# Kernel tuning notes

Hardware: AMD Instinct MI355X
Metric: run time of the kernel (lower is better)

## Reference

```python
import jax, jax.numpy as jnp
import numpy as np
import math

N_HEADS = 12
ROPE_DIM = 64
BASE = 10000.0


def _rope_tables(seq_len, dim):
    inv_freq = 1.0 / (BASE ** (jnp.arange(0, dim, 2, dtype=jnp.float32) / dim))
    t = jnp.arange(seq_len, dtype=jnp.float32)
    freqs = jnp.outer(t, inv_freq)                      # [S, dim/2]
    emb = jnp.concatenate([freqs, freqs], axis=-1)      # [S, dim]
    # broadcast shape [1, S, 1, dim]
    return jnp.cos(emb)[None, :, None, :], jnp.sin(emb)[None, :, None, :]


def _rotate_half(x):
    x1, x2 = jnp.split(x, 2, axis=-1)
    return jnp.concatenate([-x2, x1], axis=-1)


def setup_inputs() -> dict:
    key = jax.random.key(0)
    ks = jax.random.split(key, 9)
    B, S, E = 2, 2048, 768
    s = 1.0 / math.sqrt(E)
    return {
        "x": jax.random.normal(ks[0], (B, S, E), jnp.float32),
        "Wq": jax.random.normal(ks[1], (E, E), jnp.float32) * s,
        "bq": jax.random.normal(ks[2], (E,), jnp.float32) * 0.02,
        "Wk": jax.random.normal(ks[3], (E, E), jnp.float32) * s,
        "bk": jax.random.normal(ks[4], (E,), jnp.float32) * 0.02,
        "Wv": jax.random.normal(ks[5], (E, E), jnp.float32) * s,
        "bv": jax.random.normal(ks[6], (E,), jnp.float32) * 0.02,
        "Wp": jax.random.normal(ks[7], (E, E), jnp.float32) * s,
        "bp": jax.random.normal(ks[8], (E,), jnp.float32) * 0.02,
    }


def reference(x, Wq, bq, Wk, bk, Wv, bv, Wp, bp):
    B, S, E = x.shape
    H = N_HEADS
    D = E // H

    q = (x @ Wq + bq).reshape(B, S, H, D)
    k = (x @ Wk + bk).reshape(B, S, H, D)
    v = (x @ Wv + bv).reshape(B, S, H, D)

    # rotary on first ROPE_DIM dims (here ROPE_DIM == D, so full rotary)
    cos, sin = _rope_tables(S, ROPE_DIM)
    q_rot, q_pass = q[..., :ROPE_DIM], q[..., ROPE_DIM:]
    k_rot, k_pass = k[..., :ROPE_DIM], k[..., ROPE_DIM:]
    q_rot = q_rot * cos + _rotate_half(q_rot) * sin
    k_rot = k_rot * cos + _rotate_half(k_rot) * sin
    q = jnp.concatenate([q_rot, q_pass], axis=-1)
    k = jnp.concatenate([k_rot, k_pass], axis=-1)

    # scores [B, M, N, H]; mask before scaling (as in the torch code; -inf unchanged)
    att = jnp.einsum("bmhd,bnhd->bmnh", q, k)
    causal = jnp.tril(jnp.ones((S, S), dtype=bool))[None, :, :, None]
    att = jnp.where(causal, att, -jnp.inf)
    att = jax.nn.softmax(att / math.sqrt(D), axis=2)
    out = jnp.einsum("bmnh,bnhd->bmhd", att, v)

    return out.reshape(B, S, E) @ Wp + bp
```

## Files before the change

### kernel.cpp

```cpp
#include <hip/hip_runtime.h>
#include <stdint.h>

#define S_LEN 2048
#define EMB   768
#define NH    12
#define DH    64
#define M_TOT 4096
#define WELEM 589824
#define QELEM 3145728

typedef float  floatx4 __attribute__((ext_vector_type(4)));
typedef __bf16 bf16x8  __attribute__((ext_vector_type(8)));
typedef __bf16 bf16x4  __attribute__((ext_vector_type(4)));
typedef unsigned short ushortx4 __attribute__((ext_vector_type(4)));

__device__ __forceinline__ unsigned short f2bf(float f) {
    union { float f; unsigned u; } v; v.f = f;
    unsigned u = v.u;
    unsigned r = (u + 0x7FFFu + ((u >> 16) & 1u)) >> 16;
    return (unsigned short)r;
}

__device__ __forceinline__ void gl_lds16(const void* g, void* l) {
    __builtin_amdgcn_global_load_lds(
        (__attribute__((address_space(1))) const void*)g,
        (__attribute__((address_space(3))) void*)l, 16, 0, 0);
}

__global__ void cvt_all_kernel(const float* __restrict__ x, unsigned short* __restrict__ xb,
                               const float* __restrict__ W0, const float* __restrict__ W1,
                               const float* __restrict__ W2, const float* __restrict__ W3,
                               unsigned short* __restrict__ WT_all) {
    __shared__ float t[64][65];
    const int blk = blockIdx.x;
    if (blk < 3072) {
        int i = (blk * 256 + threadIdx.x) * 4;
        float4 v = *(const float4*)(x + i);
        ushortx4 r = { f2bf(v.x), f2bf(v.y), f2bf(v.z), f2bf(v.w) };
        *(ushortx4*)(xb + i) = r;
        return;
    }
    const int tc = blk - 3072;
    const int z = tc / 144, rr0 = tc % 144;
    const float* W = (z == 0) ? W0 : (z == 1 ? W1 : (z == 2 ? W2 : W3));
    unsigned short* O = WT_all + (size_t)z * WELEM;
    const int k0 = (rr0 % 12) * 64, n0 = (rr0 / 12) * 64;
    const int c = threadIdx.x & 63, r4 = threadIdx.x >> 6;
#pragma unroll
    for (int rr = 0; rr < 64; rr += 4) {
        int r = rr + r4;
        t[r][c] = W[(size_t)(k0 + r) * EMB + n0 + c];
    }
    __syncthreads();
#pragma unroll
    for (int rr = 0; rr < 64; rr += 4) {
        int nn = rr + r4;
        O[(size_t)(n0 + nn) * EMB + k0 + c] = f2bf(t[c][nn]);
    }
}

static __device__ __forceinline__ void gemm_core_128x128(
    const unsigned short* __restrict__ A, const unsigned short* __restrict__ BT,
    int m0, int n0, int K, int tid, floatx4 (&acc)[4][4],
    unsigned short* Als, unsigned short* Bls)
{
    const int lane = tid & 63;
    const int c0 = lane & 15, quad = lane >> 4;
    const int wave = tid >> 6;
    const int wm = (wave >> 1) * 64, wn = (wave & 1) * 64;

    for (int k0 = 0; k0 < K; k0 += 64) {
        __syncthreads();
#pragma unroll
        for (int it = 0; it < 4; ++it) {
            int ch = it * 256 + tid;
            int row = ch >> 3, sc = ch & 7;
            int cc = sc ^ (row & 7);
            gl_lds16(A  + (size_t)(m0 + row) * K + k0 + cc * 8, Als + ch * 8);
            gl_lds16(BT + (size_t)(n0 + row) * K + k0 + cc * 8, Bls + ch * 8);
        }
        __syncthreads();
        bf16x8 af[4][2], bfv[4][2];
#pragma unroll
        for (int ii = 0; ii < 4; ++ii) {
            int row = wm + 16 * ii + c0;
#pragma unroll
            for (int h = 0; h < 2; ++h)
                af[ii][h] = *(const bf16x8*)(Als + row * 64 + (((4 * h + quad) ^ (row & 7)) * 8));
        }
#pragma unroll
        for (int jj = 0; jj < 4; ++jj) {
            int row = wn + 16 * jj + c0;
#pragma unroll
            for (int h = 0; h < 2; ++h)
                bfv[jj][h] = *(const bf16x8*)(Bls + row * 64 + (((4 * h + quad) ^ (row & 7)) * 8));
        }
#pragma unroll
        for (int ii = 0; ii < 4; ++ii)
#pragma unroll
            for (int jj = 0; jj < 4; ++jj) {
                acc[ii][jj] = __builtin_amdgcn_mfma_f32_16x16x32_bf16(af[ii][0], bfv[jj][0], acc[ii][jj], 0, 0, 0);
                acc[ii][jj] = __builtin_amdgcn_mfma_f32_16x16x32_bf16(af[ii][1], bfv[jj][1], acc[ii][jj], 0, 0, 0);
            }
    }
}

__global__ __launch_bounds__(256, 2) void qkv_kernel(
    const unsigned short* __restrict__ xb, const unsigned short* __restrict__ WT_all,
    const float* __restrict__ bq, const float* __restrict__ bk, const float* __restrict__ bv,
    unsigned short* __restrict__ qkv_out)
{
    __shared__ __align__(16) unsigned short Als[128 * 64];
    __shared__ __align__(16) unsigned short Bls[128 * 64];
    const int z = blockIdx.z;
    const float* bias = (z == 0) ? bq : (z == 1 ? bk : bv);
    __bf16* Cout = (__bf16*)(qkv_out + (size_t)z * QELEM);
    const int m0 = blockIdx.x * 128, n0 = blockIdx.y * 128;
    const int tid = threadIdx.x, lane = tid & 63, c0 = lane & 15, quad = lane >> 4, wave = tid >> 6;
    const int wm = (wave >> 1) * 64, wn = (wave & 1) * 64;

    floatx4 acc[4][4] = {};
    gemm_core_128x128(xb, WT_all + (size_t)z * WELEM, m0, n0, EMB, tid, acc, Als, Bls);

#pragma unroll
    for (int ii = 0; ii < 4; ++ii) {
#pragma unroll
        for (int r = 0; r < 4; ++r) {
            int m = m0 + wm + 16 * ii + quad * 4 + r;
            int b = m >> 11, s = m & (S_LEN - 1);
            float vals[4];
#pragma unroll
            for (int jj = 0; jj < 4; ++jj) vals[jj] = acc[ii][jj][r] + bias[n0 + wn + 16 * jj + c0];
            if (z < 2) {
#pragma unroll
                for (int jj = 0; jj < 2; ++jj) {
                    int d = 16 * jj + c0;
                    float f = exp2f((float)d * -0.41524101186092034f);
                    float th = (float)s * f;
                    float sn, cs; sincosf(th, &sn, &cs);
                    float lo = vals[jj], hi = vals[jj + 2];
                    vals[jj]     = lo * cs - hi * sn;
                    vals[jj + 2] = hi * cs + lo * sn;
                }
            }
            if (z == 0) {
#pragma unroll
                for (int jj = 0; jj < 4; ++jj) vals[jj] *= 0.18033688011112042f;
            }
#pragma unroll
            for (int jj = 0; jj < 4; ++jj) {
                int n = n0 + wn + 16 * jj + c0;
                int h = n >> 6, d = n & 63;
                if (z < 2)
                    Cout[((size_t)(b * NH + h) * S_LEN + s) * DH + d] = (__bf16)vals[jj];
                else
                    Cout[((size_t)(b * NH + h) * DH + d) * S_LEN + s] = (__bf16)vals[jj];
            }
        }
    }
}

__global__ __launch_bounds__(256, 2) void flash_kernel(
    const unsigned short* __restrict__ Qg, const unsigned short* __restrict__ Kg,
    const unsigned short* __restrict__ Vt, unsigned short* __restrict__ Og)
{
    __shared__ __align__(16) unsigned short Kls[2][64 * 64];
    __shared__ __align__(16) unsigned short Vls[2][64 * 64];
    __shared__ __align__(16) unsigned short Pls[4][16 * 72];

    const int i = blockIdx.x;
    const int kk = i >> 8, g = i & 255;
    const int r0 = (kk == 0) ? g : (kk == 1 ? 511 - g : 512 + g);
    const int qt = 31 - r0 / 24;
    const int bh = r0 % 24;
    const int b = bh / NH, h = bh % NH;
    const int m0 = qt * 64;
    const int tid = threadIdx.x, lane = tid & 63, wave = tid >> 6;
    const int c0 = lane & 15, quad = lane >> 4;
    const size_t base = (size_t)bh * S_LEN * DH;
    const int mrow = m0 + wave * 16 + c0;

    bf16x8 qf0 = *(const bf16x8*)(Qg + base + (size_t)mrow * DH + quad * 8);
    bf16x8 qf1 = *(const bf16x8*)(Qg + base + (size_t)mrow * DH + 32 + quad * 8);

    floatx4 oa[4] = {};
    float l_lane = 0.f;
    const float C = 23.083120654223414f;
    const int ntiles = qt + 1;

#pragma unroll
    for (int it = 0; it < 2; ++it) {
        int ch = it * 256 + tid;
        int row = ch >> 3, cc = (ch & 7) ^ (row & 7);
        gl_lds16(Kg + base + (size_t)row * DH + cc * 8, &Kls[0][ch * 8]);
        gl_lds16(Vt + base + (size_t)row * S_LEN + cc * 8, &Vls[0][ch * 8]);
    }

    for (int nt = 0; nt < ntiles; ++nt) {
        __syncthreads();
        if (nt + 1 < ntiles) {
            int n0 = (nt + 1) * 64, buf = (nt + 1) & 1;
#pragma unroll
            for (int it = 0; it < 2; ++it) {
                int ch = it * 256 + tid;
                int row = ch >> 3, cc = (ch & 7) ^ (row & 7);
                gl_lds16(Kg + base + (size_t)(n0 + row) * DH + cc * 8, &Kls[buf][ch * 8]);
                gl_lds16(Vt + base + (size_t)row * S_LEN + n0 + cc * 8, &Vls[buf][ch * 8]);
            }
        }
        const unsigned short* Kb = Kls[nt & 1];
        const unsigned short* Vb = Vls[nt & 1];

        floatx4 sa[4];
        const floatx4 zz = { 0.f, 0.f, 0.f, 0.f };
#pragma unroll
        for (int jj = 0; jj < 4; ++jj) {
            int row = 16 * jj + c0;
            bf16x8 k0 = *(const bf16x8*)(Kb + row * 64 + ((quad ^ (row & 7)) * 8));
            bf16x8 k1 = *(const bf16x8*)(Kb + row * 64 + (((4 + quad) ^ (row & 7)) * 8));
            sa[jj] = __builtin_amdgcn_mfma_f32_16x16x32_bf16(k0, qf0, zz, 0, 0, 0);
            sa[jj] = __builtin_amdgcn_mfma_f32_16x16x32_bf16(k1, qf1, sa[jj], 0, 0, 0);
        }
        if (nt == ntiles - 1) {
#pragma unroll
            for (int jj = 0; jj < 4; ++jj) {
                int nb = m0 + 16 * jj + quad * 4;
#pragma unroll
                for (int rr = 0; rr < 4; ++rr)
                    if (nb + rr > mrow) sa[jj][rr] = -1e30f;
            }
        }
#pragma unroll
        for (int jj = 0; jj < 4; ++jj) {
            bf16x4 pw;
#pragma unroll
            for (int rr = 0; rr < 4; ++rr) {
                float p = __builtin_amdgcn_exp2f(sa[jj][rr] - C);
                l_lane += p;
                pw[rr] = (__bf16)p;
            }
            *(bf16x4*)(&Pls[wave][c0 * 72 + 16 * jj + quad * 4]) = pw;
        }
#pragma unroll
        for (int h2 = 0; h2 < 2; ++h2) {
            bf16x8 pf = *(const bf16x8*)(&Pls[wave][c0 * 72 + 32 * h2 + quad * 8]);
#pragma unroll
            for (int dt = 0; dt < 4; ++dt) {
                int row = 16 * dt + c0;
                bf16x8 vf = *(const bf16x8*)(Vb + row * 64 + (((4 * h2 + quad) ^ (row & 7)) * 8));
                oa[dt] = __builtin_amdgcn_mfma_f32_16x16x32_bf16(vf, pf, oa[dt], 0, 0, 0);
            }
        }
    }

    l_lane += __shfl_xor(l_lane, 16, 64);
    l_lane += __shfl_xor(l_lane, 32, 64);
    const float rl = 1.0f / l_lane;
    __bf16* Ob16 = (__bf16*)Og;
#pragma unroll
    for (int dt = 0; dt < 4; ++dt) {
        bf16x4 ov;
#pragma unroll
        for (int rr = 0; rr < 4; ++rr) ov[rr] = (__bf16)(oa[dt][rr] * rl);
        *(bf16x4*)(Ob16 + ((size_t)(b * S_LEN + mrow)) * EMB + h * DH + dt * 16 + quad * 4) = ov;
    }
}

__global__ __launch_bounds__(256, 2) void proj_kernel(
    const unsigned short* __restrict__ Ob, const unsigned short* __restrict__ WpT,
    const float* __restrict__ bp, float* __restrict__ out)
{
    __shared__ __align__(16) unsigned short Als[128 * 64];
    __shared__ __align__(16) unsigned short Bls[128 * 64];
    const int m0 = blockIdx.x * 128, n0 = blockIdx.y * 128;
    const int tid = threadIdx.x, lane = tid & 63, c0 = lane & 15, quad = lane >> 4, wave = tid >> 6;
    const int wm = (wave >> 1) * 64, wn = (wave & 1) * 64;

    floatx4 acc[4][4] = {};
    gemm_core_128x128(Ob, WpT, m0, n0, EMB, tid, acc, Als, Bls);

#pragma unroll
    for (int ii = 0; ii < 4; ++ii)
#pragma unroll
        for (int r = 0; r < 4; ++r) {
            int m = m0 + wm + 16 * ii + quad * 4 + r;
#pragma unroll
            for (int jj = 0; jj < 4; ++jj) {
                int n = n0 + wn + 16 * jj + c0;
                out[(size_t)m * EMB + n] = acc[ii][jj][r] + bp[n];
            }
        }
}

extern "C" void kernel_launch(void* const* d_in, const int* in_sizes, int n_in,
                              void* d_out, int out_size, void* d_ws, size_t ws_size,
                              hipStream_t stream)
{
    (void)in_sizes; (void)n_in; (void)out_size;
    const float* x  = (const float*)d_in[0];
    const float* Wq = (const float*)d_in[1];
    const float* bq = (const float*)d_in[2];
    const float* Wk = (const float*)d_in[3];
    const float* bk = (const float*)d_in[4];
    const float* Wv = (const float*)d_in[5];
    const float* bv = (const float*)d_in[6];
    const float* Wp = (const float*)d_in[7];
    const float* bp = (const float*)d_in[8];

    unsigned short* ws  = (unsigned short*)d_ws;
    unsigned short* xb  = ws;
    unsigned short* WT  = xb + (size_t)QELEM;
    unsigned short* QKV = WT + 4 * (size_t)WELEM;
    unsigned short* Ob  = QKV + 3 * (size_t)QELEM;
    if (ws_size < ((size_t)QELEM * 5 + 4 * (size_t)WELEM) * 2) return;

    cvt_all_kernel<<<3648, 256, 0, stream>>>(x, xb, Wq, Wk, Wv, Wp, WT);
    qkv_kernel<<<dim3(32, 6, 3), 256, 0, stream>>>(xb, WT, bq, bk, bv, QKV);
    flash_kernel<<<dim3(768), 256, 0, stream>>>(QKV, QKV + QELEM, QKV + 2 * (size_t)QELEM, Ob);
    proj_kernel<<<dim3(32, 6), 256, 0, stream>>>(Ob, WT + 3 * (size_t)WELEM, bp, (float*)d_out);
}
```

Baseline: 160.7 us.

## Split long causal query tiles across KV chunks with a separate combine kernel

The flash kernel now splits the KV range of later query tiles (16-23 into 3 chunks, 24-31 into 4) across separate blocks, writing unnormalized fp32 partial outputs and row sums to workspace. A new combine kernel sums the partials and normalizes them into the bf16 output. Because the softmax uses a fixed max constant, partials can simply be added. This is meant to balance the causal workload across more blocks (1728 instead of 768) and shorten the critical path, at the cost of an extra launch and fp32 partial traffic.

```diff
diff --git a/kernel.cpp b/kernel.cpp
--- a/kernel.cpp
+++ b/kernel.cpp
@@ -8,6 +8,7 @@
 #define M_TOT 4096
 #define WELEM 589824
 #define QELEM 3145728
+#define NSLOT 1536
 
 typedef float  floatx4 __attribute__((ext_vector_type(4)));
 typedef __bf16 bf16x8  __attribute__((ext_vector_type(8)));
@@ -162,50 +163,56 @@
 
 __global__ __launch_bounds__(256, 2) void flash_kernel(
     const unsigned short* __restrict__ Qg, const unsigned short* __restrict__ Kg,
-    const unsigned short* __restrict__ Vt, unsigned short* __restrict__ Og)
+    const unsigned short* __restrict__ Vt, unsigned short* __restrict__ Og,
+    float* __restrict__ Opart, float* __restrict__ lpart)
 {
     __shared__ __align__(16) unsigned short Kls[2][64 * 64];
     __shared__ __align__(16) unsigned short Vls[2][64 * 64];
     __shared__ __align__(16) unsigned short Pls[4][16 * 72];
 
-    const int i = blockIdx.x;
-    const int kk = i >> 8, g = i & 255;
-    const int r0 = (kk == 0) ? g : (kk == 1 ? 511 - g : 512 + g);
-    const int qt = 31 - r0 / 24;
-    const int bh = r0 % 24;
+    const int B = blockIdx.x;
+    const int bh = B / 72, j = B % 72;
+    int qt, c, nch;
+    if (j < 16)      { qt = j; c = 0; nch = 1; }
+    else if (j < 40) { int u = j - 16; qt = 16 + u / 3; c = u % 3; nch = 3; }
+    else             { int u = j - 40; qt = 24 + u / 4; c = u % 4; nch = 4; }
+    const int T = qt + 1;
+    const int cbase = T / nch, crem = T - cbase * nch;
+    const int cnt   = cbase + (c < crem ? 1 : 0);
+    const int start = c * cbase + (c < crem ? c : crem);
+
     const int b = bh / NH, h = bh % NH;
     const int m0 = qt * 64;
     const int tid = threadIdx.x, lane = tid & 63, wave = tid >> 6;
     const int c0 = lane & 15, quad = lane >> 4;
-    const size_t base = (size_t)bh * S_LEN * DH;
+    const size_t gbase = (size_t)bh * S_LEN * DH;
     const int mrow = m0 + wave * 16 + c0;
 
-    bf16x8 qf0 = *(const bf16x8*)(Qg + base + (size_t)mrow * DH + quad * 8);
-    bf16x8 qf1 = *(const bf16x8*)(Qg + base + (size_t)mrow * DH + 32 + quad * 8);
+    bf16x8 qf0 = *(const bf16x8*)(Qg + gbase + (size_t)mrow * DH + quad * 8);
+    bf16x8 qf1 = *(const bf16x8*)(Qg + gbase + (size_t)mrow * DH + 32 + quad * 8);
 
     floatx4 oa[4] = {};
     float l_lane = 0.f;
     const float C = 23.083120654223414f;
-    const int ntiles = qt + 1;
 
 #pragma unroll
     for (int it = 0; it < 2; ++it) {
         int ch = it * 256 + tid;
         int row = ch >> 3, cc = (ch & 7) ^ (row & 7);
-        gl_lds16(Kg + base + (size_t)row * DH + cc * 8, &Kls[0][ch * 8]);
-        gl_lds16(Vt + base + (size_t)row * S_LEN + cc * 8, &Vls[0][ch * 8]);
-    }
-
-    for (int nt = 0; nt < ntiles; ++nt) {
+        gl_lds16(Kg + gbase + (size_t)(start * 64 + row) * DH + cc * 8, &Kls[start & 1][ch * 8]);
+        gl_lds16(Vt + gbase + (size_t)row * S_LEN + start * 64 + cc * 8, &Vls[start & 1][ch * 8]);
+    }
+
+    for (int nt = start; nt < start + cnt; ++nt) {
         __syncthreads();
-        if (nt + 1 < ntiles) {
+        if (nt + 1 < start + cnt) {
             int n0 = (nt + 1) * 64, buf = (nt + 1) & 1;
 #pragma unroll
             for (int it = 0; it < 2; ++it) {
                 int ch = it * 256 + tid;
                 int row = ch >> 3, cc = (ch & 7) ^ (row & 7);
-                gl_lds16(Kg + base + (size_t)(n0 + row) * DH + cc * 8, &Kls[buf][ch * 8]);
-                gl_lds16(Vt + base + (size_t)row * S_LEN + n0 + cc * 8, &Vls[buf][ch * 8]);
+                gl_lds16(Kg + gbase + (size_t)(n0 + row) * DH + cc * 8, &Kls[buf][ch * 8]);
+                gl_lds16(Vt + gbase + (size_t)row * S_LEN + n0 + cc * 8, &Vls[buf][ch * 8]);
             }
         }
         const unsigned short* Kb = Kls[nt & 1];
@@ -221,7 +228,7 @@
             sa[jj] = __builtin_amdgcn_mfma_f32_16x16x32_bf16(k0, qf0, zz, 0, 0, 0);
             sa[jj] = __builtin_amdgcn_mfma_f32_16x16x32_bf16(k1, qf1, sa[jj], 0, 0, 0);
         }
-        if (nt == ntiles - 1) {
+        if (nt == qt) {
 #pragma unroll
             for (int jj = 0; jj < 4; ++jj) {
                 int nb = m0 + 16 * jj + quad * 4;
@@ -255,14 +262,61 @@
 
     l_lane += __shfl_xor(l_lane, 16, 64);
     l_lane += __shfl_xor(l_lane, 32, 64);
-    const float rl = 1.0f / l_lane;
+
+    if (nch == 1) {
+        const float rl = 1.0f / l_lane;
+        __bf16* Ob16 = (__bf16*)Og;
+#pragma unroll
+        for (int dt = 0; dt < 4; ++dt) {
+            bf16x4 ov;
+#pragma unroll
+            for (int rr = 0; rr < 4; ++rr) ov[rr] = (__bf16)(oa[dt][rr] * rl);
+            *(bf16x4*)(Ob16 + ((size_t)(b * S_LEN + mrow)) * EMB + h * DH + dt * 16 + quad * 4) = ov;
+        }
+    } else {
+        const int slot = (bh * 16 + (qt - 16)) * 4 + c;
+        const int mloc = wave * 16 + c0;
+        if (quad == 0) lpart[slot * 64 + mloc] = l_lane;
+        float* Op = Opart + (size_t)slot * 4096;
+#pragma unroll
+        for (int dt = 0; dt < 4; ++dt)
+#pragma unroll
+            for (int rr = 0; rr < 4; ++rr)
+                Op[(dt * 16 + quad * 4 + rr) * 64 + mloc] = oa[dt][rr];
+    }
+}
+
+__global__ void flash_combine_kernel(const float* __restrict__ Opart,
+                                     const float* __restrict__ lpart,
+                                     unsigned short* __restrict__ Og)
+{
+    const int bid = blockIdx.x;
+    const int bh = bid / 16, qg = bid % 16, qt = 16 + qg;
+    const int nch = (qt < 24) ? 3 : 4;
+    const int b = bh / NH, h = bh % NH;
+    const int tid = threadIdx.x;
+    const int m = tid >> 2, dseg = tid & 3;
+    const int slot0 = (bh * 16 + qg) * 4;
+    float lsum = 0.f;
+#pragma unroll
+    for (int cc = 0; cc < 4; ++cc)
+        if (cc < nch) lsum += lpart[(slot0 + cc) * 64 + m];
+    const float rl = 1.0f / lsum;
     __bf16* Ob16 = (__bf16*)Og;
-#pragma unroll
-    for (int dt = 0; dt < 4; ++dt) {
+    const size_t orow = ((size_t)(b * S_LEN + qt * 64 + m)) * EMB + h * DH + dseg * 16;
+#pragma unroll
+    for (int i = 0; i < 16; i += 4) {
         bf16x4 ov;
 #pragma unroll
-        for (int rr = 0; rr < 4; ++rr) ov[rr] = (__bf16)(oa[dt][rr] * rl);
-        *(bf16x4*)(Ob16 + ((size_t)(b * S_LEN + mrow)) * EMB + h * DH + dt * 16 + quad * 4) = ov;
+        for (int k = 0; k < 4; ++k) {
+            int d = dseg * 16 + i + k;
+            float o = 0.f;
+#pragma unroll
+            for (int cc = 0; cc < 4; ++cc)
+                if (cc < nch) o += Opart[(size_t)(slot0 + cc) * 4096 + d * 64 + m];
+            ov[k] = (__bf16)(o * rl);
+        }
+        *(bf16x4*)(Ob16 + orow + i) = ov;
     }
 }
 
@@ -312,10 +366,16 @@
     unsigned short* WT  = xb + (size_t)QELEM;
     unsigned short* QKV = WT + 4 * (size_t)WELEM;
     unsigned short* Ob  = QKV + 3 * (size_t)QELEM;
-    if (ws_size < ((size_t)QELEM * 5 + 4 * (size_t)WELEM) * 2) return;
+    float* Opart = (float*)(Ob + (size_t)QELEM);
+    float* lpart = Opart + (size_t)NSLOT * 4096;
+    size_t need = ((size_t)QELEM * 5 + 4 * (size_t)WELEM) * 2
+                + ((size_t)NSLOT * 4096 + (size_t)NSLOT * 64) * 4;
+    if (ws_size < need) return;
 
     cvt_all_kernel<<<3648, 256, 0, stream>>>(x, xb, Wq, Wk, Wv, Wp, WT);
     qkv_kernel<<<dim3(32, 6, 3), 256, 0, stream>>>(xb, WT, bq, bk, bv, QKV);
-    flash_kernel<<<dim3(768), 256, 0, stream>>>(QKV, QKV + QELEM, QKV + 2 * (size_t)QELEM, Ob);
+    flash_kernel<<<dim3(1728), 256, 0, stream>>>(QKV, QKV + QELEM, QKV + 2 * (size_t)QELEM,
+                                                 Ob, Opart, lpart);
+    flash_combine_kernel<<<dim3(384), 256, 0, stream>>>(Opart, lpart, Ob);
     proj_kernel<<<dim3(32, 6), 256, 0, stream>>>(Ob, WT + 3 * (size_t)WELEM, bp, (float*)d_out);
 }
```

New measurement: 175.0 us. 8.9% more time.

## Enlarge flash attention query tile to 128 rows per block

Applied to the files above, without the earlier changes.

Each wave now handles two 16-row query strips (128 query rows per block instead of 64), so every K/V tile staged in LDS feeds twice as many MFMAs. The grid halves to 384 blocks, and the zig-zag causal load-balancing order is replaced by a simple descending-qt order. The goal is to cut global K/V traffic and LDS loads per unit of compute. The cost is more registers and LDS per block, fewer blocks to spread over CUs, and masked work on two diagonal tiles. The launch bound is raised to 3 blocks per CU.

```diff
diff --git a/kernel.cpp b/kernel.cpp
--- a/kernel.cpp
+++ b/kernel.cpp
@@ -160,40 +160,42 @@
     }
 }
 
-__global__ __launch_bounds__(256, 2) void flash_kernel(
+__global__ __launch_bounds__(256, 3) void flash_kernel(
     const unsigned short* __restrict__ Qg, const unsigned short* __restrict__ Kg,
     const unsigned short* __restrict__ Vt, unsigned short* __restrict__ Og)
 {
     __shared__ __align__(16) unsigned short Kls[2][64 * 64];
     __shared__ __align__(16) unsigned short Vls[2][64 * 64];
-    __shared__ __align__(16) unsigned short Pls[4][16 * 72];
-
-    const int i = blockIdx.x;
-    const int kk = i >> 8, g = i & 255;
-    const int r0 = (kk == 0) ? g : (kk == 1 ? 511 - g : 512 + g);
-    const int qt = 31 - r0 / 24;
-    const int bh = r0 % 24;
+    __shared__ __align__(16) unsigned short Pls[4][32 * 72];
+
+    const int blk = blockIdx.x;
+    const int qt = 15 - (blk / 24);
+    const int bh = blk % 24;
     const int b = bh / NH, h = bh % NH;
-    const int m0 = qt * 64;
+    const int m0 = qt * 128;
     const int tid = threadIdx.x, lane = tid & 63, wave = tid >> 6;
     const int c0 = lane & 15, quad = lane >> 4;
-    const size_t base = (size_t)bh * S_LEN * DH;
-    const int mrow = m0 + wave * 16 + c0;
-
-    bf16x8 qf0 = *(const bf16x8*)(Qg + base + (size_t)mrow * DH + quad * 8);
-    bf16x8 qf1 = *(const bf16x8*)(Qg + base + (size_t)mrow * DH + 32 + quad * 8);
-
-    floatx4 oa[4] = {};
-    float l_lane = 0.f;
+    const size_t gbase = (size_t)bh * S_LEN * DH;
+    const int mrow0 = m0 + wave * 32 + c0;
+    const int mrow1 = mrow0 + 16;
+
+    bf16x8 qf[2][2];
+    qf[0][0] = *(const bf16x8*)(Qg + gbase + (size_t)mrow0 * DH + quad * 8);
+    qf[0][1] = *(const bf16x8*)(Qg + gbase + (size_t)mrow0 * DH + 32 + quad * 8);
+    qf[1][0] = *(const bf16x8*)(Qg + gbase + (size_t)mrow1 * DH + quad * 8);
+    qf[1][1] = *(const bf16x8*)(Qg + gbase + (size_t)mrow1 * DH + 32 + quad * 8);
+
+    floatx4 oa[2][4] = {};
+    float l_lane[2] = { 0.f, 0.f };
     const float C = 23.083120654223414f;
-    const int ntiles = qt + 1;
+    const int ntiles = 2 * qt + 2;
 
 #pragma unroll
     for (int it = 0; it < 2; ++it) {
         int ch = it * 256 + tid;
         int row = ch >> 3, cc = (ch & 7) ^ (row & 7);
-        gl_lds16(Kg + base + (size_t)row * DH + cc * 8, &Kls[0][ch * 8]);
-        gl_lds16(Vt + base + (size_t)row * S_LEN + cc * 8, &Vls[0][ch * 8]);
+        gl_lds16(Kg + gbase + (size_t)row * DH + cc * 8, &Kls[0][ch * 8]);
+        gl_lds16(Vt + gbase + (size_t)row * S_LEN + cc * 8, &Vls[0][ch * 8]);
     }
 
     for (int nt = 0; nt < ntiles; ++nt) {
@@ -204,65 +206,80 @@
             for (int it = 0; it < 2; ++it) {
                 int ch = it * 256 + tid;
                 int row = ch >> 3, cc = (ch & 7) ^ (row & 7);
-                gl_lds16(Kg + base + (size_t)(n0 + row) * DH + cc * 8, &Kls[buf][ch * 8]);
-                gl_lds16(Vt + base + (size_t)row * S_LEN + n0 + cc * 8, &Vls[buf][ch * 8]);
+                gl_lds16(Kg + gbase + (size_t)(n0 + row) * DH + cc * 8, &Kls[buf][ch * 8]);
+                gl_lds16(Vt + gbase + (size_t)row * S_LEN + n0 + cc * 8, &Vls[buf][ch * 8]);
             }
         }
         const unsigned short* Kb = Kls[nt & 1];
         const unsigned short* Vb = Vls[nt & 1];
 
-        floatx4 sa[4];
+        floatx4 sa[2][4];
         const floatx4 zz = { 0.f, 0.f, 0.f, 0.f };
 #pragma unroll
         for (int jj = 0; jj < 4; ++jj) {
             int row = 16 * jj + c0;
             bf16x8 k0 = *(const bf16x8*)(Kb + row * 64 + ((quad ^ (row & 7)) * 8));
             bf16x8 k1 = *(const bf16x8*)(Kb + row * 64 + (((4 + quad) ^ (row & 7)) * 8));
-            sa[jj] = __builtin_amdgcn_mfma_f32_16x16x32_bf16(k0, qf0, zz, 0, 0, 0);
-            sa[jj] = __builtin_amdgcn_mfma_f32_16x16x32_bf16(k1, qf1, sa[jj], 0, 0, 0);
-        }
-        if (nt == ntiles - 1) {
+#pragma unroll
+            for (int s = 0; s < 2; ++s) {
+                sa[s][jj] = __builtin_amdgcn_mfma_f32_16x16x32_bf16(k0, qf[s][0], zz, 0, 0, 0);
+                sa[s][jj] = __builtin_amdgcn_mfma_f32_16x16x32_bf16(k1, qf[s][1], sa[s][jj], 0, 0, 0);
+            }
+        }
+        if (nt >= ntiles - 2) {
+            int nb0 = nt * 64 + quad * 4;
+#pragma unroll
+            for (int s = 0; s < 2; ++s) {
+                int mr = mrow0 + s * 16;
+#pragma unroll
+                for (int jj = 0; jj < 4; ++jj)
+#pragma unroll
+                    for (int rr = 0; rr < 4; ++rr)
+                        if (nb0 + 16 * jj + rr > mr) sa[s][jj][rr] = -1e30f;
+            }
+        }
+#pragma unroll
+        for (int s = 0; s < 2; ++s)
 #pragma unroll
             for (int jj = 0; jj < 4; ++jj) {
-                int nb = m0 + 16 * jj + quad * 4;
-#pragma unroll
-                for (int rr = 0; rr < 4; ++rr)
-                    if (nb + rr > mrow) sa[jj][rr] = -1e30f;
-            }
-        }
-#pragma unroll
-        for (int jj = 0; jj < 4; ++jj) {
-            bf16x4 pw;
-#pragma unroll
-            for (int rr = 0; rr < 4; ++rr) {
-                float p = __builtin_amdgcn_exp2f(sa[jj][rr] - C);
-                l_lane += p;
-                pw[rr] = (__bf16)p;
-            }
-            *(bf16x4*)(&Pls[wave][c0 * 72 + 16 * jj + quad * 4]) = pw;
-        }
+                bf16x4 pw;
+#pragma unroll
+                for (int rr = 0; rr < 4; ++rr) {
+                    float p = __builtin_amdgcn_exp2f(sa[s][jj][rr] - C);
+                    l_lane[s] += p;
+                    pw[rr] = (__bf16)p;
+                }
+                *(bf16x4*)(&Pls[wave][(s * 16 + c0) * 72 + 16 * jj + quad * 4]) = pw;
+            }
 #pragma unroll
         for (int h2 = 0; h2 < 2; ++h2) {
-            bf16x8 pf = *(const bf16x8*)(&Pls[wave][c0 * 72 + 32 * h2 + quad * 8]);
+            bf16x8 pf0 = *(const bf16x8*)(&Pls[wave][c0 * 72 + 32 * h2 + quad * 8]);
+            bf16x8 pf1 = *(const bf16x8*)(&Pls[wave][(16 + c0) * 72 + 32 * h2 + quad * 8]);
 #pragma unroll
             for (int dt = 0; dt < 4; ++dt) {
                 int row = 16 * dt + c0;
                 bf16x8 vf = *(const bf16x8*)(Vb + row * 64 + (((4 * h2 + quad) ^ (row & 7)) * 8));
-                oa[dt] = __builtin_amdgcn_mfma_f32_16x16x32_bf16(vf, pf, oa[dt], 0, 0, 0);
-            }
-        }
-    }
-
-    l_lane += __shfl_xor(l_lane, 16, 64);
-    l_lane += __shfl_xor(l_lane, 32, 64);
-    const float rl = 1.0f / l_lane;
+                oa[0][dt] = __builtin_amdgcn_mfma_f32_16x16x32_bf16(vf, pf0, oa[0][dt], 0, 0, 0);
+                oa[1][dt] = __builtin_amdgcn_mfma_f32_16x16x32_bf16(vf, pf1, oa[1][dt], 0, 0, 0);
+            }
+        }
+    }
+
     __bf16* Ob16 = (__bf16*)Og;
 #pragma unroll
-    for (int dt = 0; dt < 4; ++dt) {
-        bf16x4 ov;
-#pragma unroll
-        for (int rr = 0; rr < 4; ++rr) ov[rr] = (__bf16)(oa[dt][rr] * rl);
-        *(bf16x4*)(Ob16 + ((size_t)(b * S_LEN + mrow)) * EMB + h * DH + dt * 16 + quad * 4) = ov;
+    for (int s = 0; s < 2; ++s) {
+        float l = l_lane[s];
+        l += __shfl_xor(l, 16, 64);
+        l += __shfl_xor(l, 32, 64);
+        const float rl = 1.0f / l;
+        const int mr = mrow0 + s * 16;
+#pragma unroll
+        for (int dt = 0; dt < 4; ++dt) {
+            bf16x4 ov;
+#pragma unroll
+            for (int rr = 0; rr < 4; ++rr) ov[rr] = (__bf16)(oa[s][dt][rr] * rl);
+            *(bf16x4*)(Ob16 + ((size_t)(b * S_LEN + mr)) * EMB + h * DH + dt * 16 + quad * 4) = ov;
+        }
     }
 }
 
@@ -316,6 +333,6 @@
 
     cvt_all_kernel<<<3648, 256, 0, stream>>>(x, xb, Wq, Wk, Wv, Wp, WT);
     qkv_kernel<<<dim3(32, 6, 3), 256, 0, stream>>>(xb, WT, bq, bk, bv, QKV);
-    flash_kernel<<<dim3(768), 256, 0, stream>>>(QKV, QKV + QELEM, QKV + 2 * (size_t)QELEM, Ob);
+    flash_kernel<<<dim3(384), 256, 0, stream>>>(QKV, QKV + QELEM, QKV + 2 * (size_t)QELEM, Ob);
     proj_kernel<<<dim3(32, 6), 256, 0, stream>>>(Ob, WT + 3 * (size_t)WELEM, bp, (float*)d_out);
 }
```

New measurement: 168.8 us. 1.05x slower.
